# Kernel optimization log

Measured on AMD Instinct MI355X. Metric: run time of the kernel, lower is better.

Reference implementation:

```python
import jax, jax.numpy as jnp
import numpy as np

DIM = 768
HEADS = 12
HD = DIM // HEADS
L = 196
N = 128


def layernorm(x, g, b, eps=1e-5):
    x32 = x.astype(jnp.float32)
    mu = jnp.mean(x32, axis=-1, keepdims=True)
    var = jnp.mean(jnp.square(x32 - mu), axis=-1, keepdims=True)
    return ((x32 - mu) * jax.lax.rsqrt(var + eps) * g + b).astype(x.dtype)


def setup_inputs() -> dict:
    key = jax.random.key(0)
    ks = jax.random.split(key, 16)
    s_lin = 1.0 / np.sqrt(DIM)
    s_hd = 1.0 / np.sqrt(HD)
    return {
        "x": jax.random.normal(ks[0], (L, N, DIM), jnp.float32),
        "cls": jax.random.normal(ks[1], (1, N, DIM), jnp.float32),
        "g1": jnp.ones((DIM,), jnp.float32),
        "b1": jnp.zeros((DIM,), jnp.float32),
        "g2": jnp.ones((DIM,), jnp.float32),
        "b2": jnp.zeros((DIM,), jnp.float32),
        "Wq": jax.random.uniform(ks[2], (DIM, DIM), jnp.float32, -s_lin, s_lin),
        "Wk": jax.random.uniform(ks[3], (DIM, DIM), jnp.float32, -s_lin, s_lin),
        "Wv": jax.random.uniform(ks[4], (DIM, DIM), jnp.float32, -s_lin, s_lin),
        "p1_w1": jax.random.uniform(ks[5], (HD, HD), jnp.float32, -s_hd, s_hd),
        "p1_b1": jax.random.uniform(ks[6], (HD,), jnp.float32, -s_hd, s_hd),
        "p1_w2": jax.random.uniform(ks[7], (HD, HD), jnp.float32, -s_hd, s_hd),
        "p1_b2": jax.random.uniform(ks[8], (HD,), jnp.float32, -s_hd, s_hd),
        "fc_w": jax.random.uniform(ks[9], (DIM, DIM), jnp.float32, -s_lin, s_lin),
        "fc_b": jax.random.uniform(ks[10], (DIM,), jnp.float32, -s_lin, s_lin),
        "proj_w": jax.random.uniform(ks[11], (DIM, DIM), jnp.float32, -s_lin, s_lin),
        "proj_b": jax.random.uniform(ks[12], (DIM,), jnp.float32, -s_lin, s_lin),
    }


def reference(x, cls, g1, b1, g2, b2, Wq, Wk, Wv, p1_w1, p1_b1, p1_w2, p1_b2, fc_w, fc_b, proj_w, proj_b):
    scale = HD ** (-0.5)
    xx = layernorm(jnp.concatenate([cls, x], axis=0), g1, b1)  # [L+1, N, D]
    q0 = xx[:1]   # [1, N, D] (residual)
    kv = xx[1:]   # [L, N, D]
    # torch nn.Linear: y = x @ W.T; B=1 hard-wired, keys flattened to L*N tokens
    q = (q0 @ Wq.T).reshape(1, N, HEADS, HD).transpose(0, 2, 1, 3)        # [1,H,N,hd]
    k = (kv @ Wk.T).reshape(1, L * N, HEADS, HD).transpose(0, 2, 1, 3)    # [1,H,LN,hd]
    v = (kv @ Wv.T).reshape(1, L * N, HEADS, HD).transpose(0, 2, 1, 3)    # [1,H,LN,hd]
    scores = jnp.einsum('bhqd,bhkd->bhqk', q, k) * scale                  # [1,H,N,LN]
    attn = jax.nn.softmax(scores, axis=-1)
    # predictor gate: MLP -> mean over head_dim -> softmax over singleton axis (=1)
    temq = jnp.tanh(jax.nn.relu(q @ p1_w1.T + p1_b1) @ p1_w2.T + p1_b2)   # [1,H,N,hd]
    temq = jnp.mean(temq, axis=-1, keepdims=True)                          # [1,H,N,1]
    temq = jax.nn.softmax(temq, axis=-1)                                   # ones (faithful)
    attn = (temq - 0.5) * attn
    ctx = jnp.einsum('bhqk,bhkd->bhqd', attn, v)                           # [1,H,N,hd]
    ctx = ctx.transpose(0, 2, 1, 3).reshape(1, N, DIM)
    q1 = q0 + ctx
    h = layernorm(q1, g2, b2)
    m = h @ fc_w.T + fc_b
    m = m * jax.nn.sigmoid(1.702 * m)  # QuickGELU
    m = m @ proj_w.T + proj_b
    return q1 + m  # [1, N, D]
```

## Files before the change

kernel.cpp:

```cpp
#include <hip/hip_runtime.h>

#define DIM 768
#define HEADS 12
#define HD 64
#define NB 128
#define ROWS_ALL 25216
#define ROWS_KV  25088
#define NCHUNK 64

typedef __attribute__((ext_vector_type(8))) short short8;
typedef __attribute__((ext_vector_type(4))) short short4v;
typedef __attribute__((ext_vector_type(4))) float f32x4;
typedef __attribute__((ext_vector_type(4))) unsigned int uint4v;
typedef long long i64;
typedef __attribute__((ext_vector_type(2))) long long i64x2;

__device__ __forceinline__ unsigned short f2bf(float f) {
  union { float f; unsigned u; } a; a.f = f;
  return (unsigned short)((a.u + 0x7fffu + ((a.u >> 16) & 1u)) >> 16);
}
__device__ __forceinline__ float bf2f(unsigned short u) {
  union { unsigned u; float f; } a; a.u = ((unsigned)u) << 16;
  return a.f;
}
__device__ __forceinline__ unsigned pk_fp8x4(float a, float b, float c, float d) {
  int p = __builtin_amdgcn_cvt_pk_fp8_f32(a, b, 0, false);
  p = __builtin_amdgcn_cvt_pk_fp8_f32(c, d, p, true);
  return (unsigned)p;
}

__device__ __forceinline__ void gload16(const void* g, void* l) {
  __builtin_amdgcn_global_load_lds(
      (__attribute__((address_space(1))) void*)g,
      (__attribute__((address_space(3))) void*)l, 16, 0, 0);
}

__global__ __launch_bounds__(256) void ln1_cast(
    const float* __restrict__ x, const float* __restrict__ cls,
    const float* __restrict__ g, const float* __restrict__ b,
    unsigned char* __restrict__ xx8, float* __restrict__ q0f,
    const float* __restrict__ Wq, const float* __restrict__ Wk,
    const float* __restrict__ Wv, const float* __restrict__ fcw,
    const float* __restrict__ pw,
    unsigned char* __restrict__ w8, unsigned short* __restrict__ wbf)
{
  int blk = blockIdx.x, tid = threadIdx.x;
  if (blk < ROWS_ALL / 4) {
    int row = blk * 4 + (tid >> 6);
    int lane = tid & 63;
    const float* src = (row < NB) ? (cls + (size_t)row * DIM)
                                  : (x + (size_t)(row - NB) * DIM);
    float4 v[3];
    float s = 0.f;
#pragma unroll
    for (int i = 0; i < 3; ++i) {
      v[i] = ((const float4*)src)[lane + 64 * i];
      s += v[i].x + v[i].y + v[i].z + v[i].w;
    }
#pragma unroll
    for (int o = 32; o; o >>= 1) s += __shfl_xor(s, o);
    float mean = s * (1.f / 768.f);
    float ss = 0.f;
#pragma unroll
    for (int i = 0; i < 3; ++i) {
      float a0 = v[i].x - mean, a1 = v[i].y - mean, a2 = v[i].z - mean, a3 = v[i].w - mean;
      ss += a0 * a0 + a1 * a1 + a2 * a2 + a3 * a3;
    }
#pragma unroll
    for (int o = 32; o; o >>= 1) ss += __shfl_xor(ss, o);
    float rs = rsqrtf(ss * (1.f / 768.f) + 1e-5f);
#pragma unroll
    for (int i = 0; i < 3; ++i) {
      int c4 = lane + 64 * i;
      float4 gv = ((const float4*)g)[c4];
      float4 bv = ((const float4*)b)[c4];
      float o0 = (v[i].x - mean) * rs * gv.x + bv.x;
      float o1 = (v[i].y - mean) * rs * gv.y + bv.y;
      float o2 = (v[i].z - mean) * rs * gv.z + bv.z;
      float o3 = (v[i].w - mean) * rs * gv.w + bv.w;
      ((unsigned*)(xx8 + (size_t)row * DIM))[c4] = pk_fp8x4(o0, o1, o2, o3);
      if (row < NB) {
        float4 fo; fo.x = o0; fo.y = o1; fo.z = o2; fo.w = o3;
        ((float4*)(q0f + (size_t)row * DIM))[c4] = fo;
      }
    }
  } else {
    int idx = blk - ROWS_ALL / 4;
    int w = idx / 576;
    int j4 = (idx % 576) * 256 + tid;
    const float* s = (w == 0) ? Wq : (w == 1) ? Wk : (w == 2) ? Wv
                   : (w == 3) ? fcw : pw;
    float4 v = ((const float4*)s)[j4];
    if (w < 3) {
      ((unsigned*)(w8 + (size_t)w * (DIM * DIM)))[j4] = pk_fp8x4(v.x, v.y, v.z, v.w);
    } else {
      ushort4 u; u.x = f2bf(v.x); u.y = f2bf(v.y); u.z = f2bf(v.z); u.w = f2bf(v.w);
      ((ushort4*)(wbf + (size_t)(w - 3) * (DIM * DIM)))[j4] = u;
    }
  }
}

__global__ __launch_bounds__(256) void gemm_fused(
    const unsigned char* __restrict__ xxkv, const unsigned char* __restrict__ Wk8,
    unsigned short* __restrict__ Kbf,
    const unsigned char* __restrict__ Wv8, unsigned short* __restrict__ Vtb,
    const unsigned char* __restrict__ xxall, const unsigned char* __restrict__ Wq8,
    unsigned short* __restrict__ Qbf)
{
  __shared__ unsigned char Asm[128 * 128];
  __shared__ unsigned char Bsm[128 * 128];
  int tid = threadIdx.x, wid = tid >> 6, lane = tid & 63;
  int l15 = lane & 15, l4 = lane >> 4;

  int nwg = gridDim.x;
  int bid = blockIdx.x;
  int q8 = nwg >> 3, r8 = nwg & 7;
  int xcd = bid & 7, rank = bid >> 3;
  int swz = (xcd < r8 ? xcd * (q8 + 1) : r8 * (q8 + 1) + (xcd - r8) * q8) + rank;

  const unsigned char *A, *Bt;
  unsigned short* C;
  int N, row0, col0;
  const int K = DIM;
  if (swz < 1176) {
    A = xxkv; Bt = Wk8; C = Kbf; N = DIM;
    row0 = (swz / 6) * 128; col0 = (swz % 6) * 128;
  } else if (swz < 2352) {
    int inner = swz - 1176;
    A = Wv8; Bt = xxkv; C = Vtb; N = ROWS_KV;
    row0 = (inner % 6) * 128; col0 = (inner / 6) * 128;
  } else {
    int inner = swz - 2352;
    A = xxall; Bt = Wq8; C = Qbf; N = DIM;
    row0 = 0; col0 = inner * 128;
  }
  float csc = (swz >= 2352) ? 0.18033688011112042f : 1.0f;

  int srow = tid >> 3;
  int sb = (tid & 7) ^ (srow & 7);
  const unsigned char* Ag = A + (size_t)(row0 + srow) * K + sb * 16;
  const unsigned char* Bg = Bt + (size_t)(col0 + srow) * K + sb * 16;
  size_t rstep32 = (size_t)32 * K;

  f32x4 acc[4][4] = {};
  int wr = (wid >> 1) * 64, wc = (wid & 1) * 64;
  const int nk = K >> 7;
  for (int t = 0; t < nk; ++t) {
    {
      const unsigned char* a0 = Ag + (size_t)t * 128;
      const unsigned char* b0 = Bg + (size_t)t * 128;
      char* la = (char*)Asm + wid * 1024;
      char* lb = (char*)Bsm + wid * 1024;
#pragma unroll
      for (int i = 0; i < 4; ++i) {
        gload16(a0 + i * rstep32, la + i * 4096);
        gload16(b0 + i * rstep32, lb + i * 4096);
      }
    }
    asm volatile("s_waitcnt vmcnt(0)" ::: "memory");
    __builtin_amdgcn_s_barrier();
    asm volatile("" ::: "memory");
#pragma unroll
    for (int h = 0; h < 2; ++h) {
      i64x2 aF[4], bF[4];
#pragma unroll
      for (int m = 0; m < 4; ++m) {
        int row = wr + m * 16 + l15;
        aF[m] = *(const i64x2*)((const char*)Asm + row * 128 +
                                ((((h << 2) | l4) ^ (row & 7)) << 4));
      }
#pragma unroll
      for (int n = 0; n < 4; ++n) {
        int row = wc + n * 16 + l15;
        bF[n] = *(const i64x2*)((const char*)Bsm + row * 128 +
                                ((((h << 2) | l4) ^ (row & 7)) << 4));
      }
      __builtin_amdgcn_s_setprio(1);
#pragma unroll
      for (int j = 0; j < 2; ++j)
#pragma unroll
        for (int m = 0; m < 4; ++m)
#pragma unroll
          for (int n = 0; n < 4; ++n)
            acc[m][n] = __builtin_amdgcn_mfma_f32_16x16x32_fp8_fp8(
                aF[m][j], bF[n][j], acc[m][n], 0, 0, 0);
      __builtin_amdgcn_s_setprio(0);
    }
    asm volatile("" ::: "memory");
    __builtin_amdgcn_s_barrier();
    asm volatile("" ::: "memory");
  }
#pragma unroll
  for (int m = 0; m < 4; ++m)
#pragma unroll
    for (int n = 0; n < 4; ++n)
#pragma unroll
      for (int r = 0; r < 4; ++r) {
        int rr = row0 + wr + m * 16 + l4 * 4 + r;
        int cc = col0 + wc + n * 16 + l15;
        C[(size_t)rr * N + cc] = f2bf(acc[m][n][r] * csc);
      }
}

template <int EPI>
__global__ __launch_bounds__(256, 2) void gemm_bt64(
    const unsigned short* __restrict__ A, const unsigned short* __restrict__ Bt,
    void* __restrict__ Cout, int M, int N, int K,
    const float* __restrict__ bias, const float* __restrict__ addsrc)
{
  __shared__ unsigned short Asm[2][128 * 64];
  __shared__ unsigned short Bsm[2][128 * 64];
  int tid = threadIdx.x, wid = tid >> 6, lane = tid & 63;
  int l15 = lane & 15, l4 = lane >> 4;
  int row0 = blockIdx.y * 128, col0 = blockIdx.x * 128;

  int srow = tid >> 3;
  int scol = ((tid & 7) ^ (srow & 7)) << 4;
  const char* Ag = (const char*)A + (size_t)(row0 + srow) * K * 2 + scol;
  const char* Bg = (const char*)Bt + (size_t)(col0 + srow) * K * 2 + scol;
  size_t rstep32 = (size_t)32 * K * 2;

#define STAGE(buf, kt) do {                                           \
    const char* a0 = Ag + (size_t)(kt) * 128;                         \
    const char* b0 = Bg + (size_t)(kt) * 128;                         \
    char* la = (char*)Asm[buf] + wid * 1024;                          \
    char* lb = (char*)Bsm[buf] + wid * 1024;                          \
    gload16(a0,                la);                                   \
    gload16(a0 + rstep32,      la + 4096);                            \
    gload16(a0 + 2 * rstep32,  la + 8192);                            \
    gload16(a0 + 3 * rstep32,  la + 12288);                           \
    gload16(b0,                lb);                                   \
    gload16(b0 + rstep32,      lb + 4096);                            \
    gload16(b0 + 2 * rstep32,  lb + 8192);                            \
    gload16(b0 + 3 * rstep32,  lb + 12288);                           \
  } while (0)

  f32x4 acc[4][4] = {};
  int wr = (wid >> 1) * 64, wc = (wid & 1) * 64;
  int nk = K >> 6;
  STAGE(0, 0);
  for (int t = 0; t < nk; ++t) {
    int cur = t & 1;
    __builtin_amdgcn_s_barrier();
    asm volatile("" ::: "memory");
    if (t + 1 < nk) {
      STAGE(cur ^ 1, t + 1);
      asm volatile("s_waitcnt vmcnt(8)" ::: "memory");
    } else {
      asm volatile("s_waitcnt vmcnt(0)" ::: "memory");
    }
    const char* Ab = (const char*)Asm[cur];
    const char* Bb = (const char*)Bsm[cur];
#pragma unroll
    for (int kk = 0; kk < 2; ++kk) {
      short8 aF[4], bF[4];
#pragma unroll
      for (int m = 0; m < 4; ++m) {
        int row = wr + m * 16 + l15;
        aF[m] = *(const short8*)(Ab + row * 128 + ((((kk << 2) | l4) ^ (row & 7)) << 4));
      }
#pragma unroll
      for (int n = 0; n < 4; ++n) {
        int row = wc + n * 16 + l15;
        bF[n] = *(const short8*)(Bb + row * 128 + ((((kk << 2) | l4) ^ (row & 7)) << 4));
      }
#pragma unroll
      for (int m = 0; m < 4; ++m)
#pragma unroll
        for (int n = 0; n < 4; ++n)
          acc[m][n] = __builtin_amdgcn_mfma_f32_16x16x32_bf16(aF[m], bF[n], acc[m][n], 0, 0, 0);
    }
    asm volatile("" ::: "memory");
  }
#undef STAGE
#pragma unroll
  for (int m = 0; m < 4; ++m)
#pragma unroll
    for (int n = 0; n < 4; ++n)
#pragma unroll
      for (int r = 0; r < 4; ++r) {
        int rr = row0 + wr + m * 16 + l4 * 4 + r;
        int cc = col0 + wc + n * 16 + l15;
        float v = acc[m][n][r];
        if (EPI == 1) {
          v += bias[cc];
          v = v / (1.f + __expf(-1.702f * v));
          ((unsigned short*)Cout)[(size_t)rr * N + cc] = f2bf(v);
        } else {
          v += bias[cc] + addsrc[(size_t)rr * N + cc];
          ((float*)Cout)[(size_t)rr * N + cc] = v;
        }
      }
}

__global__ __launch_bounds__(256, 4) void attn_partial(
    const unsigned short* __restrict__ Qb, const unsigned short* __restrict__ Kb,
    const unsigned short* __restrict__ Vt,
    unsigned short* __restrict__ Op, float* __restrict__ lp)
{
  __shared__ unsigned short Klds[2][64 * 64];
  __shared__ unsigned short Vlds[2][64 * 64];
  int tid = threadIdx.x, wid = tid >> 6, lane = tid & 63;
  int l15 = lane & 15, l4 = lane >> 4;
  int head = blockIdx.x >> 6, chunk = blockIdx.x & 63;
  int t0 = (49 * chunk) >> 3;
  int nkt = ((49 * (chunk + 1)) >> 3) - t0;

  short8 bQ[2][2];
#pragma unroll
  for (int m = 0; m < 2; ++m)
#pragma unroll
    for (int kk = 0; kk < 2; ++kk) {
      int qrow = wid * 32 + m * 16 + l15;
      bQ[m][kk] = *(const short8*)(Qb + (size_t)qrow * DIM + head * HD + kk * 32 + l4 * 8);
    }
  f32x4 accO[2][4] = {};
  float lrun[2] = { 0.f, 0.f };

  int srow = tid >> 3;
  int sblk = (tid & 7) ^ (srow & 7);
  const char* Kg = (const char*)(Kb + (size_t)(t0 * 64 + srow) * DIM + head * HD) + sblk * 16;
  const char* Vg = (const char*)(Vt + (size_t)(head * HD + srow) * ROWS_KV + t0 * 64) + sblk * 16;

#define STAGEKV(buf, kt) do {                                         \
    const char* k0 = Kg + (size_t)(kt) * 64 * DIM * 2;                \
    const char* v0 = Vg + (size_t)(kt) * 128;                         \
    char* lk = (char*)Klds[buf] + wid * 1024;                         \
    char* lv = (char*)Vlds[buf] + wid * 1024;                         \
    gload16(k0,                        lk);                           \
    gload16(k0 + (size_t)32 * DIM * 2, lk + 4096);                    \
    gload16(v0,                        lv);                           \
    gload16(v0 + (size_t)32 * ROWS_KV * 2, lv + 4096);                \
  } while (0)

  STAGEKV(0, 0);
  for (int kt = 0; kt < nkt; ++kt) {
    int cur = kt & 1;
    __builtin_amdgcn_s_barrier();
    asm volatile("" ::: "memory");
    if (kt + 1 < nkt) {
      STAGEKV(cur ^ 1, kt + 1);
      asm volatile("s_waitcnt vmcnt(4)" ::: "memory");
    } else {
      asm volatile("s_waitcnt vmcnt(0)" ::: "memory");
    }

    f32x4 sc[4][2] = {};
    __builtin_amdgcn_s_setprio(1);
#pragma unroll
    for (int kk = 0; kk < 2; ++kk) {
      short8 aK[4];
#pragma unroll
      for (int n = 0; n < 4; ++n) {
        int krow = n * 16 + l15;
        int blk = ((kk << 2) | l4) ^ (krow & 7);
        aK[n] = *(const short8*)((const char*)Klds[cur] + krow * 128 + blk * 16);
      }
#pragma unroll
      for (int n = 0; n < 4; ++n)
#pragma unroll
        for (int m = 0; m < 2; ++m)
          sc[n][m] = __builtin_amdgcn_mfma_f32_16x16x32_bf16(aK[n], bQ[m][kk], sc[n][m], 0, 0, 0);
    }
    __builtin_amdgcn_s_setprio(0);

    short8 pB[2][2];
#pragma unroll
    for (int m = 0; m < 2; ++m) {
      float rsum = 0.f;
#pragma unroll
      for (int n = 0; n < 4; ++n)
#pragma unroll
        for (int r = 0; r < 4; ++r) {
          float p;
          asm("v_exp_f32 %0, %1" : "=v"(p) : "v"(sc[n][m][r]));
          sc[n][m][r] = p;
          rsum += p;
        }
      rsum += __shfl_xor(rsum, 16);
      rsum += __shfl_xor(rsum, 32);
      lrun[m] += rsum;
#pragma unroll
      for (int kk2 = 0; kk2 < 2; ++kk2) {
        uint4v pw;
#pragma unroll
        for (int w = 0; w < 4; ++w) {
          int n = 2 * kk2 + (w >> 1);
          int r0 = (w & 1) * 2;
          unsigned int u;
          asm("v_cvt_pk_bf16_f32 %0, %1, %2"
              : "=v"(u) : "v"(sc[n][m][r0]), "v"(sc[n][m][r0 + 1]));
          pw[w] = u;
        }
        pB[m][kk2] = __builtin_bit_cast(short8, pw);
      }
    }

    __builtin_amdgcn_s_setprio(1);
#pragma unroll
    for (int kk2 = 0; kk2 < 2; ++kk2) {
      short8 aV[4];
#pragma unroll
      for (int nb = 0; nb < 4; ++nb) {
        int row = nb * 16 + l15;
        int blk1 = (kk2 << 2) | (l4 >> 1);
        int in1 = (l4 & 1) << 3;
        const char* vb = (const char*)Vlds[cur] + row * 128;
        short4v lo = *(const short4v*)(vb + (((blk1 ^ (row & 7)) << 4) | in1));
        short4v hi = *(const short4v*)(vb + ((((blk1 + 2) ^ (row & 7)) << 4) | in1));
        aV[nb] = __builtin_shufflevector(lo, hi, 0, 1, 2, 3, 4, 5, 6, 7);
      }
#pragma unroll
      for (int m = 0; m < 2; ++m)
#pragma unroll
        for (int nb = 0; nb < 4; ++nb)
          accO[m][nb] = __builtin_amdgcn_mfma_f32_16x16x32_bf16(aV[nb], pB[m][kk2], accO[m][nb], 0, 0, 0);
    }
    __builtin_amdgcn_s_setprio(0);
    asm volatile("" ::: "memory");
  }
#undef STAGEKV
  size_t pb = (size_t)(head * NCHUNK + chunk) * 128;
#pragma unroll
  for (int m = 0; m < 2; ++m) {
    int q = wid * 32 + m * 16 + l15;
#pragma unroll
    for (int nb = 0; nb < 4; ++nb) {
      ushort4 o;
      o.x = f2bf(accO[m][nb][0]); o.y = f2bf(accO[m][nb][1]);
      o.z = f2bf(accO[m][nb][2]); o.w = f2bf(accO[m][nb][3]);
      *(ushort4*)(Op + (pb + q) * 64 + nb * 16 + l4 * 4) = o;
    }
    if (l4 == 0) {
      lp[pb + q] = lrun[m];
    }
  }
}

__device__ __forceinline__ float blk_sum256(float v, volatile float* red) {
  int tid = threadIdx.x;
#pragma unroll
  for (int o = 32; o; o >>= 1) v += __shfl_xor(v, o);
  __syncthreads();
  if ((tid & 63) == 0) red[tid >> 6] = v;
  __syncthreads();
  return red[0] + red[1] + red[2] + red[3];
}

__global__ __launch_bounds__(256) void combine_ln2(
    const unsigned short* __restrict__ Op, const float* __restrict__ lp,
    const float* __restrict__ q0f, const float* __restrict__ g2, const float* __restrict__ b2,
    float* __restrict__ q1, unsigned short* __restrict__ hb)
{
  int q = blockIdx.x, tid = threadIdx.x;
  __shared__ float lS[HEADS * NCHUNK];
  __shared__ float red[4];
  for (int i = tid; i < HEADS * NCHUNK; i += 256)
    lS[i] = lp[(size_t)i * 128 + q];
  __syncthreads();
  float vals[3];
#pragma unroll
  for (int ii = 0; ii < 3; ++ii) {
    int c = tid + ii * 256;
    int h = c >> 6, d = c & 63;
    float num = 0.f, den = 0.f;
    for (int cc = 0; cc < NCHUNK; ++cc) {
      den += lS[h * NCHUNK + cc];
      num += bf2f(Op[((size_t)(h * NCHUNK + cc) * 128 + q) * 64 + d]);
    }
    float ctx = 0.5f * num / den;
    float v = q0f[(size_t)q * DIM + c] + ctx;
    q1[(size_t)q * DIM + c] = v;
    vals[ii] = v;
  }
  float s = blk_sum256(vals[0] + vals[1] + vals[2], red);
  float mean = s * (1.f / 768.f);
  float d0 = vals[0] - mean, d1 = vals[1] - mean, d2 = vals[2] - mean;
  float ss = blk_sum256(d0 * d0 + d1 * d1 + d2 * d2, red);
  float rs = rsqrtf(ss * (1.f / 768.f) + 1e-5f);
#pragma unroll
  for (int ii = 0; ii < 3; ++ii) {
    int c = tid + ii * 256;
    hb[(size_t)q * DIM + c] = f2bf((vals[ii] - mean) * rs * g2[c] + b2[c]);
  }
}

extern "C" void kernel_launch(void* const* d_in, const int* in_sizes, int n_in,
                              void* d_out, int out_size, void* d_ws, size_t ws_size,
                              hipStream_t stream) {
  const float* x   = (const float*)d_in[0];
  const float* cls = (const float*)d_in[1];
  const float* g1  = (const float*)d_in[2];
  const float* b1  = (const float*)d_in[3];
  const float* g2  = (const float*)d_in[4];
  const float* b2  = (const float*)d_in[5];
  const float* Wq  = (const float*)d_in[6];
  const float* Wk  = (const float*)d_in[7];
  const float* Wv  = (const float*)d_in[8];
  const float* fcw = (const float*)d_in[13];
  const float* fcb = (const float*)d_in[14];
  const float* pw  = (const float*)d_in[15];
  const float* pb  = (const float*)d_in[16];

  char* ws = (char*)d_ws;
  size_t off = 0;
  auto alloc = [&](size_t bytes) {
    char* p = ws + off;
    off += (bytes + 255) & ~(size_t)255;
    return p;
  };
  unsigned char*  xx8  = (unsigned char*)alloc((size_t)ROWS_ALL * DIM);
  float*          q0f  = (float*)alloc((size_t)NB * DIM * 4);
  unsigned short* Kbf  = (unsigned short*)alloc((size_t)ROWS_KV * DIM * 2);
  unsigned short* Vtb  = (unsigned short*)alloc((size_t)DIM * ROWS_KV * 2);
  unsigned short* Qbf  = (unsigned short*)alloc((size_t)NB * DIM * 2);
  unsigned char*  w8   = (unsigned char*)alloc((size_t)3 * DIM * DIM);
  unsigned short* wbf  = (unsigned short*)alloc((size_t)2 * DIM * DIM * 2);
  unsigned short* Opar = (unsigned short*)alloc((size_t)HEADS * NCHUNK * 128 * 64 * 2);
  float*          lpar = (float*)alloc((size_t)HEADS * NCHUNK * 128 * 4);
  float*          q1   = (float*)alloc((size_t)NB * DIM * 4);
  unsigned short* hb   = (unsigned short*)alloc((size_t)NB * DIM * 2);
  unsigned short* m1b  = (unsigned short*)alloc((size_t)NB * DIM * 2);

  unsigned char* Wq8 = w8;
  unsigned char* Wk8 = w8 + (size_t)1 * DIM * DIM;
  unsigned char* Wv8 = w8 + (size_t)2 * DIM * DIM;
  unsigned short* fwb = wbf;
  unsigned short* pwb = wbf + (size_t)1 * DIM * DIM;

  ln1_cast<<<ROWS_ALL / 4 + 2880, 256, 0, stream>>>(
      x, cls, g1, b1, xx8, q0f, Wq, Wk, Wv, fcw, pw, w8, wbf);

  gemm_fused<<<1176 + 1176 + 6, 256, 0, stream>>>(
      xx8 + (size_t)NB * DIM, Wk8, Kbf, Wv8, Vtb, xx8, Wq8, Qbf);

  attn_partial<<<HEADS * NCHUNK, 256, 0, stream>>>(Qbf, Kbf, Vtb, Opar, lpar);
  combine_ln2<<<NB, 256, 0, stream>>>(Opar, lpar, q0f, g2, b2, q1, hb);

  gemm_bt64<1><<<dim3(DIM / 128, 1), 256, 0, stream>>>(
      hb, fwb, m1b, NB, DIM, DIM, fcb, nullptr);
  gemm_bt64<2><<<dim3(DIM / 128, 1), 256, 0, stream>>>(
      m1b, pwb, d_out, NB, DIM, DIM, pb, q1);
}
```

Before: 132.7 us.

## Store K and Q in fp8 and use fp8 MFMA for attention scores

The projection GEMM now writes K and the pre-scaled Q as fp8 bytes instead of bf16, while V stays bf16. The attention kernel loads K tiles at half the size, with a new LDS swizzle and one fewer async load per stage, and computes QK^T with fp8 MFMA instructions. This halves K write and read traffic and the LDS footprint for K. In exchange, score precision drops, which could hurt accuracy because Q carries the softmax scale. The epilogue writes K one byte at a time, and those scattered byte stores may be inefficient.

```diff
diff --git a/kernel.cpp b/kernel.cpp
--- a/kernel.cpp
+++ b/kernel.cpp
@@ -27,6 +27,9 @@
   int p = __builtin_amdgcn_cvt_pk_fp8_f32(a, b, 0, false);
   p = __builtin_amdgcn_cvt_pk_fp8_f32(c, d, p, true);
   return (unsigned)p;
+}
+__device__ __forceinline__ unsigned char f2fp8(float v) {
+  return (unsigned char)(__builtin_amdgcn_cvt_pk_fp8_f32(v, v, 0, false) & 0xff);
 }
 
 __device__ __forceinline__ void gload16(const void* g, void* l) {
@@ -102,10 +105,10 @@
 
 __global__ __launch_bounds__(256) void gemm_fused(
     const unsigned char* __restrict__ xxkv, const unsigned char* __restrict__ Wk8,
-    unsigned short* __restrict__ Kbf,
+    unsigned char* __restrict__ K8,
     const unsigned char* __restrict__ Wv8, unsigned short* __restrict__ Vtb,
     const unsigned char* __restrict__ xxall, const unsigned char* __restrict__ Wq8,
-    unsigned short* __restrict__ Qbf)
+    unsigned char* __restrict__ Q8)
 {
   __shared__ unsigned char Asm[128 * 128];
   __shared__ unsigned char Bsm[128 * 128];
@@ -114,24 +117,25 @@
 
   int nwg = gridDim.x;
   int bid = blockIdx.x;
-  int q8 = nwg >> 3, r8 = nwg & 7;
+  int q8g = nwg >> 3, r8 = nwg & 7;
   int xcd = bid & 7, rank = bid >> 3;
-  int swz = (xcd < r8 ? xcd * (q8 + 1) : r8 * (q8 + 1) + (xcd - r8) * q8) + rank;
+  int swz = (xcd < r8 ? xcd * (q8g + 1) : r8 * (q8g + 1) + (xcd - r8) * q8g) + rank;
 
   const unsigned char *A, *Bt;
-  unsigned short* C;
+  unsigned char* C8 = nullptr;
+  unsigned short* Cb = nullptr;
   int N, row0, col0;
   const int K = DIM;
   if (swz < 1176) {
-    A = xxkv; Bt = Wk8; C = Kbf; N = DIM;
+    A = xxkv; Bt = Wk8; C8 = K8; N = DIM;
     row0 = (swz / 6) * 128; col0 = (swz % 6) * 128;
   } else if (swz < 2352) {
     int inner = swz - 1176;
-    A = Wv8; Bt = xxkv; C = Vtb; N = ROWS_KV;
+    A = Wv8; Bt = xxkv; Cb = Vtb; N = ROWS_KV;
     row0 = (inner % 6) * 128; col0 = (inner / 6) * 128;
   } else {
     int inner = swz - 2352;
-    A = xxall; Bt = Wq8; C = Qbf; N = DIM;
+    A = xxall; Bt = Wq8; C8 = Q8; N = DIM;
     row0 = 0; col0 = inner * 128;
   }
   float csc = (swz >= 2352) ? 0.18033688011112042f : 1.0f;
@@ -198,7 +202,9 @@
       for (int r = 0; r < 4; ++r) {
         int rr = row0 + wr + m * 16 + l4 * 4 + r;
         int cc = col0 + wc + n * 16 + l15;
-        C[(size_t)rr * N + cc] = f2bf(acc[m][n][r] * csc);
+        float v = acc[m][n][r] * csc;
+        if (C8) C8[(size_t)rr * N + cc] = f2fp8(v);
+        else    Cb[(size_t)rr * N + cc] = f2bf(v);
       }
 }
 
@@ -294,11 +300,11 @@
 }
 
 __global__ __launch_bounds__(256, 4) void attn_partial(
-    const unsigned short* __restrict__ Qb, const unsigned short* __restrict__ Kb,
+    const unsigned char* __restrict__ Q8, const unsigned char* __restrict__ K8,
     const unsigned short* __restrict__ Vt,
     unsigned short* __restrict__ Op, float* __restrict__ lp)
 {
-  __shared__ unsigned short Klds[2][64 * 64];
+  __shared__ unsigned char Klds[2][64 * 64];
   __shared__ unsigned short Vlds[2][64 * 64];
   int tid = threadIdx.x, wid = tid >> 6, lane = tid & 63;
   int l15 = lane & 15, l4 = lane >> 4;
@@ -306,30 +312,27 @@
   int t0 = (49 * chunk) >> 3;
   int nkt = ((49 * (chunk + 1)) >> 3) - t0;
 
-  short8 bQ[2][2];
-#pragma unroll
-  for (int m = 0; m < 2; ++m)
-#pragma unroll
-    for (int kk = 0; kk < 2; ++kk) {
-      int qrow = wid * 32 + m * 16 + l15;
-      bQ[m][kk] = *(const short8*)(Qb + (size_t)qrow * DIM + head * HD + kk * 32 + l4 * 8);
-    }
+  i64x2 bQ[2];
+#pragma unroll
+  for (int m = 0; m < 2; ++m) {
+    int qrow = wid * 32 + m * 16 + l15;
+    bQ[m] = *(const i64x2*)(Q8 + (size_t)qrow * DIM + head * HD + l4 * 16);
+  }
   f32x4 accO[2][4] = {};
   float lrun[2] = { 0.f, 0.f };
 
-  int srow = tid >> 3;
-  int sblk = (tid & 7) ^ (srow & 7);
-  const char* Kg = (const char*)(Kb + (size_t)(t0 * 64 + srow) * DIM + head * HD) + sblk * 16;
-  const char* Vg = (const char*)(Vt + (size_t)(head * HD + srow) * ROWS_KV + t0 * 64) + sblk * 16;
+  int srowK = tid >> 2;
+  int sbK = (tid & 3) ^ ((srowK >> 1) & 3);
+  const char* Kg = (const char*)(K8 + (size_t)(t0 * 64 + srowK) * DIM + head * HD) + sbK * 16;
+  int srowV = tid >> 3;
+  int sbV = (tid & 7) ^ (srowV & 7);
+  const char* Vg = (const char*)(Vt + (size_t)(head * HD + srowV) * ROWS_KV + t0 * 64) + sbV * 16;
 
 #define STAGEKV(buf, kt) do {                                         \
-    const char* k0 = Kg + (size_t)(kt) * 64 * DIM * 2;                \
+    gload16(Kg + (size_t)(kt) * 64 * DIM, (char*)Klds[buf] + wid * 1024); \
     const char* v0 = Vg + (size_t)(kt) * 128;                         \
-    char* lk = (char*)Klds[buf] + wid * 1024;                         \
     char* lv = (char*)Vlds[buf] + wid * 1024;                         \
-    gload16(k0,                        lk);                           \
-    gload16(k0 + (size_t)32 * DIM * 2, lk + 4096);                    \
-    gload16(v0,                        lv);                           \
+    gload16(v0,                            lv);                       \
     gload16(v0 + (size_t)32 * ROWS_KV * 2, lv + 4096);                \
   } while (0)
 
@@ -340,27 +343,29 @@
     asm volatile("" ::: "memory");
     if (kt + 1 < nkt) {
       STAGEKV(cur ^ 1, kt + 1);
-      asm volatile("s_waitcnt vmcnt(4)" ::: "memory");
+      asm volatile("s_waitcnt vmcnt(3)" ::: "memory");
     } else {
       asm volatile("s_waitcnt vmcnt(0)" ::: "memory");
     }
 
     f32x4 sc[4][2] = {};
     __builtin_amdgcn_s_setprio(1);
-#pragma unroll
-    for (int kk = 0; kk < 2; ++kk) {
-      short8 aK[4];
+    {
+      i64x2 aK[4];
 #pragma unroll
       for (int n = 0; n < 4; ++n) {
         int krow = n * 16 + l15;
-        int blk = ((kk << 2) | l4) ^ (krow & 7);
-        aK[n] = *(const short8*)((const char*)Klds[cur] + krow * 128 + blk * 16);
-      }
-#pragma unroll
-      for (int n = 0; n < 4; ++n)
-#pragma unroll
-        for (int m = 0; m < 2; ++m)
-          sc[n][m] = __builtin_amdgcn_mfma_f32_16x16x32_bf16(aK[n], bQ[m][kk], sc[n][m], 0, 0, 0);
+        aK[n] = *(const i64x2*)((const char*)Klds[cur] + krow * 64 +
+                                ((l4 ^ ((krow >> 1) & 3)) << 4));
+      }
+#pragma unroll
+      for (int j = 0; j < 2; ++j)
+#pragma unroll
+        for (int n = 0; n < 4; ++n)
+#pragma unroll
+          for (int m = 0; m < 2; ++m)
+            sc[n][m] = __builtin_amdgcn_mfma_f32_16x16x32_fp8_fp8(
+                aK[n][j], bQ[m][j], sc[n][m], 0, 0, 0);
     }
     __builtin_amdgcn_s_setprio(0);
 
@@ -511,9 +516,9 @@
   };
   unsigned char*  xx8  = (unsigned char*)alloc((size_t)ROWS_ALL * DIM);
   float*          q0f  = (float*)alloc((size_t)NB * DIM * 4);
-  unsigned short* Kbf  = (unsigned short*)alloc((size_t)ROWS_KV * DIM * 2);
+  unsigned char*  K8   = (unsigned char*)alloc((size_t)ROWS_KV * DIM);
   unsigned short* Vtb  = (unsigned short*)alloc((size_t)DIM * ROWS_KV * 2);
-  unsigned short* Qbf  = (unsigned short*)alloc((size_t)NB * DIM * 2);
+  unsigned char*  Q8   = (unsigned char*)alloc((size_t)NB * DIM);
   unsigned char*  w8   = (unsigned char*)alloc((size_t)3 * DIM * DIM);
   unsigned short* wbf  = (unsigned short*)alloc((size_t)2 * DIM * DIM * 2);
   unsigned short* Opar = (unsigned short*)alloc((size_t)HEADS * NCHUNK * 128 * 64 * 2);
@@ -532,9 +537,9 @@
       x, cls, g1, b1, xx8, q0f, Wq, Wk, Wv, fcw, pw, w8, wbf);
 
   gemm_fused<<<1176 + 1176 + 6, 256, 0, stream>>>(
-      xx8 + (size_t)NB * DIM, Wk8, Kbf, Wv8, Vtb, xx8, Wq8, Qbf);
-
-  attn_partial<<<HEADS * NCHUNK, 256, 0, stream>>>(Qbf, Kbf, Vtb, Opar, lpar);
+      xx8 + (size_t)NB * DIM, Wk8, K8, Wv8, Vtb, xx8, Wq8, Q8);
+
+  attn_partial<<<HEADS * NCHUNK, 256, 0, stream>>>(Q8, K8, Vtb, Opar, lpar);
   combine_ln2<<<NB, 256, 0, stream>>>(Opar, lpar, q0f, g2, b2, q1, hb);
 
   gemm_bt64<1><<<dim3(DIM / 128, 1), 256, 0, stream>>>(
```

New measurement: 132.4 us. No clear change (-0.2%).
